# Performance work log

Hardware: AMD Instinct MI355X
Metric: run time of the kernel (lower is better)

The kernel has to match this reference:

```python
import jax, jax.numpy as jnp
import numpy as np

N_QUBITS = 11   # state dim 2**11 = 2048
N_LAYERS = 6
BATCH = 8192


def _rz(phi):
    # RZ(phi) = diag(e^{-i phi/2}, e^{+i phi/2}); phi scalar -> (2,2), phi (B,) -> (B,2,2)
    e = jnp.exp(-0.5j * phi.astype(jnp.complex64))
    z = jnp.zeros_like(e)
    return jnp.stack([jnp.stack([e, z], -1), jnp.stack([z, jnp.conj(e)], -1)], -2)


def _ry(theta):
    # RY(theta) = [[cos t, -sin t], [sin t, cos t]], t = theta/2
    t = 0.5 * theta.astype(jnp.float32)
    c = jnp.cos(t).astype(jnp.complex64)
    s = jnp.sin(t).astype(jnp.complex64)
    return jnp.stack([jnp.stack([c, -s], -1), jnp.stack([s, c], -1)], -2)


def _apply_1q(state, U, q, n):
    # state: (B, 2**n); qubit q is the q-th most-significant bit of the ket index
    B = state.shape[0]
    st = state.reshape(B, 2 ** q, 2, 2 ** (n - 1 - q))
    if U.ndim == 2:   # shared (trainable) gate
        st = jnp.einsum('ab,sxby->sxay', U, st)
    else:             # per-sample (data-encoding) gate, U: (B,2,2)
        st = jnp.einsum('sab,sxby->sxay', U, st)
    return st.reshape(B, 2 ** n)


def _apply_cnot(state, c, n):
    # CNOT with control c, target c+1 (adjacent in the chain)
    B = state.shape[0]
    st = state.reshape(B, 2 ** c, 2, 2, 2 ** (n - 2 - c))
    st = jnp.stack([st[:, :, 0], st[:, :, 1, ::-1]], axis=2)  # flip target when control=1
    return st.reshape(B, 2 ** n)


def _forward(X, params):
    n, L = N_QUBITS, N_LAYERS
    B = X.shape[0]
    # pad/truncate features to n_qubits (matches build_circuit)
    Xe = X[:, :n] if X.shape[1] >= n else jnp.pad(X, ((0, 0), (0, n - X.shape[1])))
    state = jnp.zeros((B, 2 ** n), jnp.complex64).at[:, 0].set(1.0)  # |0...0>
    for l in range(L):
        for q in range(n):
            state = _apply_1q(state, _rz(params[l, q, 0]), q, n)
            state = _apply_1q(state, _ry(params[l, q, 1]), q, n)
            state = _apply_1q(state, _rz(params[l, q, 2]), q, n)
            if l == L - 1:  # data re-upload RY only on the last layer (per source)
                state = _apply_1q(state, _ry(Xe[:, q]), q, n)
        if n > 1:
            for c in range(n - 1):
                state = _apply_cnot(state, c, n)
    return state  # (B, 2**n) complex64


def setup_inputs() -> dict:
    key = jax.random.key(0)
    k1, k2 = jax.random.split(key)
    X = jax.random.uniform(k1, (BATCH, N_QUBITS), jnp.float32) * (2.0 * np.pi)
    params = jax.random.normal(k2, (N_LAYERS, N_QUBITS, 3), jnp.float32) * 0.01
    return {"X": X, "params": params}


def reference(X, params):
    state = _forward(X, params)
    # return real/imag stacked so the output is a real float32 array
    return jnp.stack([state.real, state.imag], -1)  # (B, 2**n, 2)
```

## Files before the change

### kernel.cpp

```cpp
#include <hip/hip_runtime.h>
#include <math.h>

#define NQ   11
#define DIM  2048
#define NL   6

typedef float v2f __attribute__((ext_vector_type(2)));

__host__ __device__ constexpr int swzA(int x) {
    return x ^ ((x >> 6) & 31) ^ ((x & 2) << 3) ^ ((x & 1) << 3);
}
__host__ __device__ constexpr int hperm(int x) {
    return x ^ (x>>1) ^ (x>>2) ^ (x>>3) ^ (x>>4) ^ (x>>5)
             ^ (x>>6) ^ (x>>7) ^ (x>>8) ^ (x>>9) ^ (x>>10);
}

__device__ __forceinline__ float2 cfma2(float2 u, float2 a, float2 v, float2 b) {
    float2 r;
    r.x = u.x*a.x - u.y*a.y + v.x*b.x - v.y*b.y;
    r.y = u.x*a.y + u.y*a.x + v.x*b.y + v.y*b.x;
    return r;
}

template<int CTRL>
__device__ __forceinline__ v2f dpp_xor(v2f v) {
    const int x = __builtin_amdgcn_update_dpp(
        0, __float_as_int(v.x), CTRL, 0xF, 0xF, true);
    const int y = __builtin_amdgcn_update_dpp(
        0, __float_as_int(v.y), CTRL, 0xF, 0xF, true);
    v2f r; r.x = __int_as_float(x); r.y = __int_as_float(y);
    return r;
}

__global__ __launch_bounds__(256) void qnn_shared_kernel(
    const float* __restrict__ P,
    float2* __restrict__ ws)
{
    __shared__ float2 lds[DIM];
    __shared__ float2 G[NL*NQ][4];
    const int t = threadIdx.x;

    if (t < NL*NQ) {
        const float p0 = P[t*3+0], p1 = P[t*3+1], p2 = P[t*3+2];
        const float th = 0.5f*p1;
        const float c  = cosf(th), s = sinf(th);
        const float al = 0.5f*(p0+p2), be = 0.5f*(p0-p2);
        const float ca = cosf(al), sa = sinf(al);
        const float cb = cosf(be), sb = sinf(be);
        G[t][0] = make_float2( c*ca, -c*sa);
        G[t][1] = make_float2(-s*cb, -s*sb);
        G[t][2] = make_float2( s*cb, -s*sb);
        G[t][3] = make_float2( c*ca,  c*sa);
    }

    const int a0w = swzA(t);
    const int a1b = swzA(((t>>5)<<8) | (t&31));
    const int a2b = swzA(((t>>2)<<5) | (t&3));
    const int a3b = swzA(t ^ (t>>1));
    const int natb = ((t>>2)<<5) | (t&3);

    float2 a[8];
    #pragma unroll
    for (int k = 0; k < 8; ++k) a[k] = make_float2(0.f, 0.f);
    if (t == 0) a[0] = make_float2(1.f, 0.f);
    __syncthreads();

    #define CG(g_, rb_) { \
        const float2 U00=G[g_][0], U01=G[g_][1], U10=G[g_][2], U11=G[g_][3]; \
        _Pragma("unroll") \
        for (int kk = 0; kk < 8; ++kk) if (!(kk & (rb_))) { \
            const float2 a0 = a[kk], a1 = a[kk|(rb_)]; \
            a[kk]       = cfma2(U00, a0, U01, a1); \
            a[kk|(rb_)] = cfma2(U10, a0, U11, a1); \
        } }

    #define SG(g_, m_, b_) { \
        const float2 ca_ = (b_) ? G[g_][3] : G[g_][0]; \
        const float2 cb_ = (b_) ? G[g_][2] : G[g_][1]; \
        _Pragma("unroll") \
        for (int kk = 0; kk < 8; ++kk) { \
            float2 p; \
            p.x = __shfl_xor(a[kk].x, m_); \
            p.y = __shfl_xor(a[kk].y, m_); \
            a[kk] = cfma2(ca_, a[kk], cb_, p); \
        } }

    for (int l = 0; l < NL; ++l) {
        const int g0 = l*NQ;
        CG(g0+0, 4) CG(g0+1, 2) CG(g0+2, 1)

        #pragma unroll
        for (int k = 0; k < 8; ++k) lds[a0w ^ swzA(k<<8)] = a[k];
        __syncthreads();
        #pragma unroll
        for (int k = 0; k < 8; ++k) a[k] = lds[a1b ^ swzA(k<<5)];
        __syncthreads();
        CG(g0+3, 4) CG(g0+4, 2) CG(g0+5, 1)

        #pragma unroll
        for (int k = 0; k < 8; ++k) lds[a1b ^ swzA(k<<5)] = a[k];
        __syncthreads();
        #pragma unroll
        for (int k = 0; k < 8; ++k) a[k] = lds[a2b ^ swzA(k<<2)];
        __syncthreads();
        CG(g0+6, 4) CG(g0+7, 2) CG(g0+8, 1)

        SG(g0+9, 2, (t>>1)&1)
        SG(g0+10, 1, t&1)

        if (l < NL-1) {
            #pragma unroll
            for (int k = 0; k < 8; ++k) lds[a2b ^ swzA(k<<2)] = a[k];
            __syncthreads();
            #pragma unroll
            for (int k = 0; k < 8; ++k)
                a[k] = lds[a3b ^ swzA((k<<8) ^ (k<<7))];
            __syncthreads();
        } else {
            #pragma unroll
            for (int k = 0; k < 8; ++k) ws[natb | (k<<2)] = a[k];
        }
    }
    #undef CG
    #undef SG
}

__global__ __launch_bounds__(128, 4) void qnn_last_kernel(
    const float* __restrict__ X,
    const float4* __restrict__ S5c,
    float4* __restrict__ out4)
{
    __shared__ float4 ldsc[DIM/2];
    __shared__ float2 gc[NQ];
    const int b = blockIdx.x;
    const int t = threadIdx.x;

    if (t < NQ) {
        const float tx = 0.5f * X[(size_t)b*NQ + t];
        gc[t] = make_float2(cosf(tx), sinf(tx));
    }

    v2f a[16];
    #pragma unroll
    for (int k = 0; k < 8; ++k) {
        const float4 v = S5c[(k<<7) | t];
        a[2*k]   = (v2f){v.x, v.y};
        a[2*k+1] = (v2f){v.z, v.w};
    }
    __syncthreads();

    #define RG(q_, rb_) { \
        const float c = gc[q_].x, sn = gc[q_].y; \
        const v2f cc = {c, c}, sv = {sn, sn}; \
        _Pragma("unroll") \
        for (int j = 0; j < 16; ++j) if (!(j & (rb_))) { \
            const v2f a0 = a[j], a1 = a[j|(rb_)]; \
            a[j]       = cc*a0 - sv*a1; \
            a[j|(rb_)] = sv*a0 + cc*a1; \
        } }

    #define CGD(q_, CTRL_, r_) { \
        const float c = gc[q_].x, sn = gc[q_].y; \
        const float sg = (r_) ? sn : -sn; \
        const v2f cc = {c, c}, sgv = {sg, sg}; \
        _Pragma("unroll") \
        for (int k = 0; k < 8; ++k) { \
            const v2f o0 = a[2*k], o1 = a[2*k+1]; \
            const v2f p0 = dpp_xor<CTRL_>(o1); \
            const v2f p1 = dpp_xor<CTRL_>(o0); \
            a[2*k]   = cc*o0 + sgv*p0; \
            a[2*k+1] = cc*o1 + sgv*p1; \
        } }

    RG(0, 8) RG(1, 4) RG(2, 2) RG(10, 1)

    #pragma unroll
    for (int k = 0; k < 8; ++k)
        ldsc[(k<<7) | t] = make_float4(a[2*k].x, a[2*k].y, a[2*k+1].x, a[2*k+1].y);
    __syncthreads();
    const int cR = ((t>>4)<<7) | (t & 15);
    #pragma unroll
    for (int k = 0; k < 8; ++k) {
        const float4 v = ldsc[cR | (k<<4)];
        a[2*k]   = (v2f){v.x, v.y};
        a[2*k+1] = (v2f){v.z, v.w};
    }
    RG(3, 8) RG(4, 4) RG(5, 2)
    __syncthreads();

    {
        const int sB    = (((t>>4)&7)<<8) | (((t>>1)&7)<<2) | ((t&1)<<1);
        const int cellB = hperm(sB) >> 1;
        const int pt    = __popc(t) & 1;
        #pragma unroll
        for (int k = 0; k < 8; ++k) {
            const int cell = cellB ^ (hperm(k<<5) >> 1);
            const bool sw  = (pt ^ (__popc(k) & 1)) != 0;
            const v2f lo = sw ? a[2*k+1] : a[2*k];
            const v2f hi = sw ? a[2*k]   : a[2*k+1];
            ldsc[cell] = make_float4(lo.x, lo.y, hi.x, hi.y);
        }
    }
    __syncthreads();

    #pragma unroll
    for (int k = 0; k < 8; ++k) {
        const float4 v = ldsc[(k<<7) | t];
        a[2*k]   = (v2f){v.x, v.y};
        a[2*k+1] = (v2f){v.z, v.w};
    }

    CGD(6, 0x140, ((t>>3) ^ (t>>4)) & 1)
    CGD(7, 0x141, ((t>>2) ^ (t>>3)) & 1)
    CGD(8, 27,    ((t>>1) ^ (t>>2)) & 1)
    CGD(9, 177,   ( t     ^ (t>>1)) & 1)

    float4* o = out4 + (size_t)b * (DIM/2);
    #pragma unroll
    for (int k = 0; k < 8; ++k)
        o[(k<<7) | t] = make_float4(a[2*k].x, a[2*k].y, a[2*k+1].x, a[2*k+1].y);
    #undef RG
    #undef CGD
}

extern "C" void kernel_launch(void* const* d_in, const int* in_sizes, int n_in,
                              void* d_out, int out_size, void* d_ws, size_t ws_size,
                              hipStream_t stream) {
    const float* X = (const float*)d_in[0];
    const float* P = (const float*)d_in[1];
    float2* ws  = (float2*)d_ws;
    const int B = in_sizes[0] / NQ;
    qnn_shared_kernel<<<1, 256, 0, stream>>>(P, ws);
    qnn_last_kernel<<<B, 128, 0, stream>>>(X, (const float4*)ws, (float4*)d_out);
}
```

Measured before the change: 52.12 us.

## Widen shared-state kernel to 1024 threads using shuffle/DPP qubit gates

The single-block kernel that evolves the batch-independent state through the first layers now uses 1024 threads, each holding 2 amplitudes instead of 8. Most qubit gates are applied across lanes with shuffles and DPP, which cuts the number of LDS transposes per layer from three to two, and the final result is written with float4 stores. The aim is to shorten the serial latency of this one-block prologue kernel, at the cost of more cross-lane traffic and synchronisation over a larger block.

```diff
diff --git a/kernel.cpp b/kernel.cpp
--- a/kernel.cpp
+++ b/kernel.cpp
@@ -7,9 +7,6 @@
 
 typedef float v2f __attribute__((ext_vector_type(2)));
 
-__host__ __device__ constexpr int swzA(int x) {
-    return x ^ ((x >> 6) & 31) ^ ((x & 2) << 3) ^ ((x & 1) << 3);
-}
 __host__ __device__ constexpr int hperm(int x) {
     return x ^ (x>>1) ^ (x>>2) ^ (x>>3) ^ (x>>4) ^ (x>>5)
              ^ (x>>6) ^ (x>>7) ^ (x>>8) ^ (x>>9) ^ (x>>10);
@@ -31,10 +28,19 @@
     v2f r; r.x = __int_as_float(x); r.y = __int_as_float(y);
     return r;
 }
-
-__global__ __launch_bounds__(256) void qnn_shared_kernel(
+template<int CTRL>
+__device__ __forceinline__ float2 dpp_xor_f2(float2 v) {
+    float2 r;
+    r.x = __int_as_float(__builtin_amdgcn_update_dpp(
+        0, __float_as_int(v.x), CTRL, 0xF, 0xF, true));
+    r.y = __int_as_float(__builtin_amdgcn_update_dpp(
+        0, __float_as_int(v.y), CTRL, 0xF, 0xF, true));
+    return r;
+}
+
+__global__ __launch_bounds__(1024) void qnn_shared_kernel(
     const float* __restrict__ P,
-    float2* __restrict__ ws)
+    float4* __restrict__ ws4)
 {
     __shared__ float2 lds[DIM];
     __shared__ float2 G[NL*NQ][4];
@@ -53,76 +59,66 @@
         G[t][3] = make_float2( c*ca,  c*sa);
     }
 
-    const int a0w = swzA(t);
-    const int a1b = swzA(((t>>5)<<8) | (t&31));
-    const int a2b = swzA(((t>>2)<<5) | (t&3));
-    const int a3b = swzA(t ^ (t>>1));
-    const int natb = ((t>>2)<<5) | (t&3);
-
-    float2 a[8];
-    #pragma unroll
-    for (int k = 0; k < 8; ++k) a[k] = make_float2(0.f, 0.f);
-    if (t == 0) a[0] = make_float2(1.f, 0.f);
-    __syncthreads();
-
-    #define CG(g_, rb_) { \
-        const float2 U00=G[g_][0], U01=G[g_][1], U10=G[g_][2], U11=G[g_][3]; \
-        _Pragma("unroll") \
-        for (int kk = 0; kk < 8; ++kk) if (!(kk & (rb_))) { \
-            const float2 a0 = a[kk], a1 = a[kk|(rb_)]; \
-            a[kk]       = cfma2(U00, a0, U01, a1); \
-            a[kk|(rb_)] = cfma2(U10, a0, U11, a1); \
-        } }
-
-    #define SG(g_, m_, b_) { \
-        const float2 ca_ = (b_) ? G[g_][3] : G[g_][0]; \
-        const float2 cb_ = (b_) ? G[g_][2] : G[g_][1]; \
-        _Pragma("unroll") \
-        for (int kk = 0; kk < 8; ++kk) { \
-            float2 p; \
-            p.x = __shfl_xor(a[kk].x, m_); \
-            p.y = __shfl_xor(a[kk].y, m_); \
-            a[kk] = cfma2(ca_, a[kk], cb_, p); \
-        } }
+    const int b0 = t ^ ((t >> 6) & 15);
+    const int lin1 = (((t>>2)&15)<<6) | (((t>>6)&15)<<2) | (t&3);
+    const int b1 = lin1 ^ ((t >> 2) & 15);
+    const int gt = t ^ (t >> 1);
+    const int b2 = gt ^ ((gt >> 6) & 15);
+    const int bn = (2*t) ^ (((2*t) >> 6) & 15);
+
+    float2 a0 = make_float2(0.f, 0.f), a1 = make_float2(0.f, 0.f);
+    if (t == 0) a0 = make_float2(1.f, 0.f);
+    __syncthreads();
+
+    #define CGK(g_) { \
+        const float2 n0 = cfma2(G[g_][0], a0, G[g_][1], a1); \
+        const float2 n1 = cfma2(G[g_][2], a0, G[g_][3], a1); \
+        a0 = n0; a1 = n1; }
+
+    #define SGL(g_, m_) { \
+        const int bb = (t & (m_)) ? 1 : 0; \
+        const float2 ca_ = bb ? G[g_][3] : G[g_][0]; \
+        const float2 cb_ = bb ? G[g_][2] : G[g_][1]; \
+        float2 p; \
+        p.x = __shfl_xor(a0.x, m_); p.y = __shfl_xor(a0.y, m_); \
+        a0 = cfma2(ca_, a0, cb_, p); \
+        p.x = __shfl_xor(a1.x, m_); p.y = __shfl_xor(a1.y, m_); \
+        a1 = cfma2(ca_, a1, cb_, p); }
+
+    #define SGD(g_, CTRL_, m_) { \
+        const int bb = (t & (m_)) ? 1 : 0; \
+        const float2 ca_ = bb ? G[g_][3] : G[g_][0]; \
+        const float2 cb_ = bb ? G[g_][2] : G[g_][1]; \
+        float2 p = dpp_xor_f2<CTRL_>(a0); \
+        a0 = cfma2(ca_, a0, cb_, p); \
+        p = dpp_xor_f2<CTRL_>(a1); \
+        a1 = cfma2(ca_, a1, cb_, p); }
 
     for (int l = 0; l < NL; ++l) {
         const int g0 = l*NQ;
-        CG(g0+0, 4) CG(g0+1, 2) CG(g0+2, 1)
-
-        #pragma unroll
-        for (int k = 0; k < 8; ++k) lds[a0w ^ swzA(k<<8)] = a[k];
+        CGK(g0+0)
+        SGL(g0+5, 32) SGL(g0+6, 16) SGL(g0+7, 8) SGL(g0+8, 4)
+        SGD(g0+9, 78, 2) SGD(g0+10, 177, 1)
+
+        lds[b0] = a0; lds[b0 ^ 1024] = a1;
         __syncthreads();
-        #pragma unroll
-        for (int k = 0; k < 8; ++k) a[k] = lds[a1b ^ swzA(k<<5)];
+        a0 = lds[b1]; a1 = lds[b1 ^ 1024];
+
+        SGL(g0+1, 32) SGL(g0+2, 16) SGL(g0+3, 8) SGL(g0+4, 4)
+
+        lds[b1] = a0; lds[b1 ^ 1024] = a1;
         __syncthreads();
-        CG(g0+3, 4) CG(g0+4, 2) CG(g0+5, 1)
-
-        #pragma unroll
-        for (int k = 0; k < 8; ++k) lds[a1b ^ swzA(k<<5)] = a[k];
-        __syncthreads();
-        #pragma unroll
-        for (int k = 0; k < 8; ++k) a[k] = lds[a2b ^ swzA(k<<2)];
-        __syncthreads();
-        CG(g0+6, 4) CG(g0+7, 2) CG(g0+8, 1)
-
-        SG(g0+9, 2, (t>>1)&1)
-        SG(g0+10, 1, t&1)
-
         if (l < NL-1) {
-            #pragma unroll
-            for (int k = 0; k < 8; ++k) lds[a2b ^ swzA(k<<2)] = a[k];
-            __syncthreads();
-            #pragma unroll
-            for (int k = 0; k < 8; ++k)
-                a[k] = lds[a3b ^ swzA((k<<8) ^ (k<<7))];
+            a0 = lds[b2]; a1 = lds[b2 ^ 1544];
             __syncthreads();
         } else {
-            #pragma unroll
-            for (int k = 0; k < 8; ++k) ws[natb | (k<<2)] = a[k];
+            const float2 lo = lds[bn], hi = lds[bn ^ 1];
+            ws4[t] = make_float4(lo.x, lo.y, hi.x, hi.y);
         }
     }
-    #undef CG
-    #undef SG
+    #undef CGK
+    #undef SGL
+    #undef SGD
 }
 
 __global__ __launch_bounds__(128, 4) void qnn_last_kernel(
@@ -228,8 +224,8 @@
                               hipStream_t stream) {
     const float* X = (const float*)d_in[0];
     const float* P = (const float*)d_in[1];
-    float2* ws  = (float2*)d_ws;
+    float4* ws4 = (float4*)d_ws;
     const int B = in_sizes[0] / NQ;
-    qnn_shared_kernel<<<1, 256, 0, stream>>>(P, ws);
-    qnn_last_kernel<<<B, 128, 0, stream>>>(X, (const float4*)ws, (float4*)d_out);
-}
+    qnn_shared_kernel<<<1, 1024, 0, stream>>>(P, ws4);
+    qnn_last_kernel<<<B, 128, 0, stream>>>(X, (const float4*)ws4, (float4*)d_out);
+}
```

New measurement: 51.89 us. About the same (-0.4%).
